# Kernel tuning notes

Measured on AMD Instinct MI355X. Metric: run time of the kernel, lower is better.

## Reference

```python
import jax, jax.numpy as jnp
import numpy as np

NEG = 0.01  # leaky_relu negative slope

def leaky(x):
    return jax.nn.leaky_relu(x, NEG)

def mlp3(x, W0, b0, W1, b1, W2, b2):
    h = leaky(x @ W0 + b0)
    h = leaky(h @ W1 + b1)
    return h @ W2 + b2

B_, T_, N_FINE, F_IN = 2, 4, 64800, 78
N_COARSE, E_LAT, H, D_OUT = 842, 5894, 256, 256

def setup_inputs() -> dict:
    key = jax.random.key(0)
    ks = jax.random.split(key, 24)
    def lin(k, i, o):
        return jax.random.normal(k, (i, o), jnp.float32) * 0.02, jnp.zeros((o,), jnp.float32)
    x = jax.random.normal(ks[0], (B_, T_, N_FINE, F_IN), jnp.float32)
    # one edge per fine node: src = node index, dst = its coarse h3 cell
    edge_index = jnp.stack([jnp.arange(N_FINE, dtype=jnp.int32),
                            jax.random.randint(ks[1], (N_FINE,), 0, N_COARSE, dtype=jnp.int32)])
    edge_attr = 2.0 * jax.random.uniform(ks[2], (N_FINE, 2), jnp.float32) - 1.0  # [sin d, cos d]
    latent_edge_index = jax.random.randint(ks[3], (2, E_LAT), 0, N_COARSE, dtype=jnp.int32)
    latent_edge_attr = 2.0 * jax.random.uniform(ks[4], (E_LAT, 2), jnp.float32) - 1.0
    h3_nodes = jax.random.normal(ks[5], (N_COARSE, F_IN), jnp.float32) * 0.02
    eW0, eb0 = lin(ks[6], 2 * F_IN + 2, H); eW1, eb1 = lin(ks[7], H, H); eW2, eb2 = lin(ks[8], H, D_OUT)
    nW0, nb0 = lin(ks[9], F_IN + D_OUT, H); nW1, nb1 = lin(ks[10], H, H); nW2, nb2 = lin(ks[11], H, D_OUT)
    rW0, rb0 = lin(ks[12], 2, H); rW1, rb1 = lin(ks[13], H, H); rW2, rb2 = lin(ks[14], H, D_OUT)
    rWs, rbs = lin(ks[15], 2, D_OUT)
    return dict(x=x, edge_index=edge_index, edge_attr=edge_attr,
                latent_edge_index=latent_edge_index, latent_edge_attr=latent_edge_attr,
                h3_nodes=h3_nodes,
                eW0=eW0, eb0=eb0, eW1=eW1, eb1=eb1, eW2=eW2, eb2=eb2,
                nW0=nW0, nb0=nb0, nW1=nW1, nb1=nb1, nW2=nW2, nb2=nb2,
                rW0=rW0, rb0=rb0, rW1=rW1, rb1=rb1, rW2=rW2, rb2=rb2,
                rWs=rWs, rbs=rbs)

def reference(x, edge_index, edge_attr, latent_edge_index, latent_edge_attr, h3_nodes,
              eW0, eb0, eW1, eb1, eW2, eb2,
              nW0, nb0, nW1, nb1, nW2, nb2,
              rW0, rb0, rW1, rb1, rW2, rb2, rWs, rbs):
    b, t, n, f = x.shape
    B = b * t
    xf = x.reshape(B, n, f)                      # (b t) n f
    src, dst = edge_index[0], edge_index[1]      # [E]
    nc = h3_nodes.shape[0]
    E = src.shape[0]
    # --- edge MLP: gather src fine feats, dst latent feats, edge attrs ---
    e_in = jnp.concatenate([
        xf[:, src],                                          # [B,E,f]
        jnp.broadcast_to(h3_nodes[dst][None], (B, E, f)),    # [B,E,f]
        jnp.broadcast_to(edge_attr[None], (B, E, 2)),        # [B,E,2]
    ], axis=-1)
    msgs = mlp3(e_in, eW0, eb0, eW1, eb1, eW2, eb2)          # [B,E,D]
    # --- scatter-sum to coarse nodes ---
    agg = jax.vmap(lambda m: jax.ops.segment_sum(m, dst, num_segments=nc))(msgs)  # [B,nc,D]
    # --- node MLP on concat(latent nodes, aggregated messages) ---
    n_in = jnp.concatenate([jnp.broadcast_to(h3_nodes[None], (B, nc, f)), agg], axis=-1)
    nodes = mlp3(n_in, nW0, nb0, nW1, nb1, nW2, nb2)          # [B,nc,D]
    nodes = nodes.reshape(b, t, nc, -1)
    # --- residual MLP over latent edge attrs (eval: dropout off, parametrized skip) ---
    h = leaky(latent_edge_attr @ rW0 + rb0)
    h = leaky(h @ rW1 + rb1)
    attrs = h @ rW2 + rb2 + (latent_edge_attr @ rWs + rbs)
    return (nodes, latent_edge_index, attrs)
```

## Files before the change

### kernel.cpp

```cpp
#include <hip/hip_runtime.h>

#define E_EDGES 64800
#define NC      842
#define NB      8
#define FIN     78
#define E_LAT   5894
#define NROWS_NODE (NB*NC)
#define NTILES_E 2025
#define NODE_B   421
#define TAIL_B   192

#define OUT_IDX_OFF   1724416
#define OUT_IDX_N     11788
#define OUT_ATTR_OFF  1736204

#define AGG_OFF    0
#define CNT_OFF    6897664
#define CUR_OFF    6901032
#define SSRC_OFF   6904400
#define SDST_OFF   7163600
#define SATTR_OFF  7293200
#define WPACK_OFF  7811600

#define WOFF_E0 0
#define WOFF_E1 24576
#define WOFF_E2 90112
#define WOFF_N0 155648
#define WOFF_N1 245760
#define WOFF_N2 311296
#define WOFF_R0 376832
#define WOFF_R1 385024
#define WOFF_R2 450560

#define SH   262
#define SA_N 362

typedef __bf16 bf16x8 __attribute__((ext_vector_type(8)));
typedef float  f32x4  __attribute__((ext_vector_type(4)));

__device__ __forceinline__ unsigned short f2bf(float f) {
    unsigned u = __builtin_bit_cast(unsigned, f);
    return (unsigned short)((u + 0x7fffu + ((u >> 16) & 1u)) >> 16);
}
__device__ __forceinline__ unsigned packRTZ(float lo, float hi) {
    return __builtin_amdgcn_perm(__builtin_bit_cast(unsigned, hi),
                                 __builtin_bit_cast(unsigned, lo), 0x07060302u);
}

template<int MF>
__device__ __forceinline__ void zero_acc(f32x4 (&acc)[MF][4]) {
#pragma unroll
    for (int mf = 0; mf < MF; ++mf)
#pragma unroll
        for (int nf = 0; nf < 4; ++nf)
            acc[mf][nf] = (f32x4){0.f, 0.f, 0.f, 0.f};
}

template<int MF, int NKS>
__device__ __forceinline__ void run_layer(const unsigned short* lA, int strideA,
                                          const unsigned short* Wp, int nfg0,
                                          int m15, int q, f32x4 (&acc)[MF][4]) {
    const unsigned short* wp0 = Wp + (size_t)nfg0 * 512 + (threadIdx.x & 63) * 8;
    bf16x8 bcur[4], bnxt[4];
#pragma unroll
    for (int nf = 0; nf < 4; ++nf) bcur[nf] = *(const bf16x8*)(wp0 + nf * 512);
#pragma unroll
    for (int kk = 0; kk < NKS; ++kk) {
        if (kk + 1 < NKS) {
#pragma unroll
            for (int nf = 0; nf < 4; ++nf)
                bnxt[nf] = *(const bf16x8*)(wp0 + (size_t)(kk + 1) * 16 * 512 + nf * 512);
        }
        bf16x8 a[MF];
#pragma unroll
        for (int mf = 0; mf < MF; ++mf)
            a[mf] = *(const bf16x8*)(lA + (mf * 16 + m15) * strideA + kk * 32 + q * 8);
#pragma unroll
        for (int nf = 0; nf < 4; ++nf)
#pragma unroll
            for (int mf = 0; mf < MF; ++mf)
                acc[mf][nf] = __builtin_amdgcn_mfma_f32_16x16x32_bf16(a[mf], bcur[nf], acc[mf][nf], 0, 0, 0);
#pragma unroll
        for (int nf = 0; nf < 4; ++nf) bcur[nf] = bnxt[nf];
    }
}

template<int MF>
__device__ __forceinline__ void epi_act(unsigned short* Sb, int stride, const f32x4 (&acc)[MF][4],
                                        const float* bias, int w, int m15, int q) {
#pragma unroll
    for (int nf = 0; nf < 4; ++nf) {
        int col = w * 64 + nf * 16 + m15;
        float bv = bias[col];
#pragma unroll
        for (int mf = 0; mf < MF; ++mf)
#pragma unroll
            for (int r4 = 0; r4 < 4; ++r4) {
                int row = mf * 16 + q * 4 + r4;
                float y = acc[mf][nf][r4] + bv;
                y = fmaxf(y, 0.01f * y);
                Sb[row * stride + col] = (unsigned short)(__builtin_bit_cast(unsigned, y) >> 16);
            }
    }
}

__global__ void pack_weights(const float* s0, const float* s1, const float* s2,
                             const float* s3, const float* s4, const float* s5,
                             const float* s6, const float* s7, const float* s8,
                             unsigned short* wp) {
    const int ksA[9]  = {3, 8, 8, 11, 8, 8, 1, 8, 8};
    const int kaA[9]  = {96, 256, 256, 334, 256, 256, 2, 256, 256};
    const int offA[9] = {WOFF_E0, WOFF_E1, WOFF_E2, WOFF_N0, WOFF_N1, WOFF_N2,
                         WOFF_R0, WOFF_R1, WOFF_R2};
    const float* srcs[9] = {s0, s1, s2, s3, s4, s5, s6, s7, s8};
    int rem = blockIdx.x;
    int l = 0;
    while (rem >= ksA[l] * 16) { rem -= ksA[l] * 16; ++l; }
    int kk = rem >> 4, nf = rem & 15;
    int lane = threadIdx.x >> 3, j = threadIdx.x & 7;
    int k = kk * 32 + (lane >> 4) * 8 + j;
    int n = nf * 16 + (lane & 15);
    float v = 0.f;
    if (l == 0) {
        int sr = (k < 78) ? k : ((k < 80) ? 156 + (k - 78) : -1);
        if (sr >= 0) v = s0[sr * 256 + n];
    } else {
        v = (k < kaA[l]) ? srcs[l][k * 256 + n] : 0.f;
    }
    wp[(size_t)offA[l] + (size_t)(kk * 16 + nf) * 512 + lane * 8 + j] = f2bf(v);
}

__global__ __launch_bounds__(256) void h3mm_kernel(const float* __restrict__ h3,
                                                   const float* __restrict__ eW0,
                                                   const float* __restrict__ eb0,
                                                   float* __restrict__ h3we) {
    __shared__ float hs[16][80];
    const int tid = threadIdx.x;
    const int rbase = blockIdx.x * 16;
    for (int i = tid; i < 16 * 78; i += 256) {
        int r = i / 78, k = i % 78;
        int gr = rbase + r;
        hs[r][k] = (gr < NC) ? h3[gr * FIN + k] : 0.f;
    }
    __syncthreads();
    const int c = tid;
    float acc[16];
#pragma unroll
    for (int r = 0; r < 16; ++r) acc[r] = eb0[c];
    for (int k = 0; k < 78; ++k) {
        float wv = eW0[(78 + k) * 256 + c];
#pragma unroll
        for (int r = 0; r < 16; ++r) acc[r] = fmaf(hs[r][k], wv, acc[r]);
    }
#pragma unroll
    for (int r = 0; r < 16; ++r) {
        int gr = rbase + r;
        if (gr < NC) h3we[(size_t)gr * 256 + c] = acc[r];
    }
}

__global__ void hist_kernel(const int* __restrict__ dstA, int* __restrict__ cnt) {
    int e = blockIdx.x * 256 + threadIdx.x;
    if (e < E_EDGES) atomicAdd(&cnt[dstA[e]], 1);
}
__global__ void scan_kernel(const int* __restrict__ cnt, int* __restrict__ cursor) {
    __shared__ int s[1024];
    int t = threadIdx.x;
    s[t] = (t < NC) ? cnt[t] : 0;
    __syncthreads();
    for (int d = 1; d < 1024; d <<= 1) {
        int v = (t >= d) ? s[t - d] : 0;
        __syncthreads();
        s[t] += v;
        __syncthreads();
    }
    if (t < NC) cursor[t] = (t == 0) ? 0 : s[t - 1];
}
__global__ void scatter_kernel(const int* __restrict__ srcA, const int* __restrict__ dstA,
                               const float* __restrict__ eattr, int* __restrict__ cursor,
                               int* __restrict__ ssrc, short* __restrict__ sdst,
                               float2* __restrict__ sattr) {
    int e = blockIdx.x * 256 + threadIdx.x;
    if (e < E_EDGES) {
        int d = dstA[e];
        int p = atomicAdd(&cursor[d], 1);
        ssrc[p] = srcA[e];
        sdst[p] = (short)d;
        sattr[p] = ((const float2*)eattr)[e];
    }
}

__global__ __launch_bounds__(256, 6) void edge_mlp_kernel(
    const float* __restrict__ x, const float* __restrict__ h3we,
    const float* __restrict__ eb1, const float* __restrict__ eb2,
    const unsigned short* __restrict__ wpack, const int* __restrict__ ssrc,
    const short* __restrict__ sdst, const float2* __restrict__ sattr,
    float* __restrict__ agg) {
    __shared__ __align__(16) unsigned short S[32 * SH];
    __shared__ short dstl[32];
    __shared__ unsigned char starts[36];
    __shared__ int nseg;

    const int base = blockIdx.x * 32, b = blockIdx.y;
    const int tid = threadIdx.x, lane = tid & 63, w = tid >> 6;
    const int m15 = lane & 15, q = lane >> 4;

    if (tid < 32) dstl[tid] = sdst[base + tid];
    __syncthreads();

    if (tid == 0) {
        int ns = 0; short prev = -2;
        for (int r = 0; r < 32; ++r) {
            short d = dstl[r];
            if (d != prev) { starts[ns++] = (unsigned char)r; prev = d; }
        }
        starts[ns] = 32;
        nseg = ns;
    }

    {
        const int rr = tid >> 3, j = tid & 7;
        const int eg = base + rr;
        const float* xr = x + ((size_t)b * E_EDGES + ssrc[eg]) * FIN;
        unsigned short* Sr = S + rr * SH;
#pragma unroll
        for (int t = 0; t < 6; ++t) {
            int p = j + 8 * t;
            if (p < 39) {
                float2 f = *(const float2*)(xr + 2 * p);
                *(unsigned*)(Sr + 2 * p) = packRTZ(f.x, f.y);
            } else if (p == 39) {
                float2 a2 = sattr[eg];
                *(unsigned*)(Sr + 78) = packRTZ(a2.x, a2.y);
            } else {
                *(unsigned*)(Sr + 2 * p) = 0;
            }
        }
    }
    float bnf[4];
#pragma unroll
    for (int nf = 0; nf < 4; ++nf) bnf[nf] = eb2[w * 64 + nf * 16 + m15];
    __syncthreads();

    f32x4 acc[2][4];
    zero_acc<2>(acc);
    run_layer<2, 3>(S, SH, wpack + WOFF_E0, w * 4, m15, q, acc);
    __syncthreads();
    {
#pragma unroll
        for (int mf = 0; mf < 2; ++mf)
#pragma unroll
            for (int r4 = 0; r4 < 4; ++r4) {
                int row = mf * 16 + q * 4 + r4;
                const float* hb = h3we + (size_t)dstl[row] * 256;
#pragma unroll
                for (int nf = 0; nf < 4; ++nf) {
                    int col = w * 64 + nf * 16 + m15;
                    float y = acc[mf][nf][r4] + hb[col];
                    y = fmaxf(y, 0.01f * y);
                    S[row * SH + col] = (unsigned short)(__builtin_bit_cast(unsigned, y) >> 16);
                }
            }
    }
    __syncthreads();

    zero_acc<2>(acc);
    run_layer<2, 8>(S, SH, wpack + WOFF_E1, w * 4, m15, q, acc);
    __syncthreads();
    epi_act<2>(S, SH, acc, eb1, w, m15, q);
    __syncthreads();

    zero_acc<2>(acc);
    run_layer<2, 8>(S, SH, wpack + WOFF_E2, w * 4, m15, q, acc);

    const int ns = nseg;
#pragma unroll
    for (int nf = 0; nf < 4; ++nf) {
        for (int s = 0; s < ns; ++s) {
            const int lo = starts[s], hi = starts[s + 1];
            float t = 0.f;
#pragma unroll
            for (int mf = 0; mf < 2; ++mf)
#pragma unroll
                for (int r4 = 0; r4 < 4; ++r4) {
                    int row = mf * 16 + q * 4 + r4;
                    t += (row >= lo && row < hi) ? acc[mf][nf][r4] : 0.f;
                }
            t += __shfl_xor(t, 16, 64);
            t += __shfl_xor(t, 32, 64);
            if (q == nf) {
                int dc = dstl[lo];
                atomicAdd(&agg[((size_t)b * NC + dc) * 256 + w * 64 + nf * 16 + m15],
                          t + bnf[nf] * (float)(hi - lo));
            }
        }
    }
}

__global__ __launch_bounds__(256, 4) void node_tail_kernel(
    const float* __restrict__ h3, const float* __restrict__ agg,
    const float* __restrict__ nb0, const float* __restrict__ nb1, const float* __restrict__ nb2,
    const unsigned short* __restrict__ wpack, float* __restrict__ out,
    const float* __restrict__ la, const float* __restrict__ rb0,
    const float* __restrict__ rb1, const float* __restrict__ rb2,
    const float* __restrict__ rWs, const float* __restrict__ rbs,
    const int* __restrict__ lei) {
    __shared__ __align__(16) unsigned short S[32 * SH];

    const int tid = threadIdx.x, lane = tid & 63, w = tid >> 6;
    const int m15 = lane & 15, q = lane >> 4;

    if (blockIdx.x >= NODE_B) {
        const int blk = blockIdx.x - NODE_B;
        if (blk >= 185) {
            for (int i = (blk - 185) * 256 + tid; i < OUT_IDX_N; i += 7 * 256)
                out[OUT_IDX_OFF + i] = (float)lei[i];
            return;
        }
        const int base = blk * 32;
        {
            const int rr = tid >> 3, jj = tid & 7;
            unsigned short* Sr = S + rr * SH;
            unsigned v0 = 0;
            if (jj == 0 && base + rr < E_LAT) {
                float2 f = *(const float2*)(la + (size_t)(base + rr) * 2);
                v0 = packRTZ(f.x, f.y);
            }
            *(unsigned*)(Sr + 2 * jj) = v0;
            *(unsigned*)(Sr + 2 * (jj + 8)) = 0;
        }
        __syncthreads();

        f32x4 acc[2][4];
        zero_acc<2>(acc);
        run_layer<2, 1>(S, SH, wpack + WOFF_R0, w * 4, m15, q, acc);
        __syncthreads();
        epi_act<2>(S, SH, acc, rb0, w, m15, q);
        __syncthreads();

        zero_acc<2>(acc);
        run_layer<2, 8>(S, SH, wpack + WOFF_R1, w * 4, m15, q, acc);
        __syncthreads();
        epi_act<2>(S, SH, acc, rb1, w, m15, q);
        __syncthreads();

        zero_acc<2>(acc);
        run_layer<2, 8>(S, SH, wpack + WOFF_R2, w * 4, m15, q, acc);

        float* outA = out + OUT_ATTR_OFF;
#pragma unroll
        for (int nf = 0; nf < 4; ++nf) {
            int col = w * 64 + nf * 16 + m15;
            float bv = rb2[col] + rbs[col];
            float ws0 = rWs[col], ws1 = rWs[256 + col];
#pragma unroll
            for (int mf = 0; mf < 2; ++mf)
#pragma unroll
                for (int r4 = 0; r4 < 4; ++r4) {
                    int row = mf * 16 + q * 4 + r4;
                    int e = base + row;
                    if (e < E_LAT) {
                        float v = acc[mf][nf][r4] + bv + la[e * 2] * ws0 + la[e * 2 + 1] * ws1;
                        outA[(size_t)e * 256 + col] = v;
                    }
                }
        }
        return;
    }

    const int base = blockIdx.x * 16;

    {
        const int rr = tid >> 4, l16 = tid & 15;
        const int jj = base + rr;
        const int vl = jj < NROWS_NODE;
        const int c = vl ? jj % NC : 0;
        const float* hr = h3 + c * FIN;
        const float* ar = agg + (size_t)jj * 256;
        unsigned short* Sr = S + rr * SA_N;
#pragma unroll
        for (int tt = 0; tt < 12; ++tt) {
            int p = l16 + 16 * tt;
            if (p < 39) {
                float2 f = *(const float2*)(hr + 2 * p);
                *(unsigned*)(Sr + 2 * p) = packRTZ(f.x, f.y);
            } else if (p < 167) {
                unsigned v = 0;
                if (vl) { float2 f = *(const float2*)(ar + 2 * p - 78); v = packRTZ(f.x, f.y); }
                *(unsigned*)(Sr + 2 * p) = v;
            } else if (p < 176) {
                *(unsigned*)(Sr + 2 * p) = 0;
            }
        }
    }
    __syncthreads();

    f32x4 acc[1][4];
    zero_acc<1>(acc);
    run_layer<1, 11>(S, SA_N, wpack + WOFF_N0, w * 4, m15, q, acc);
    __syncthreads();
    epi_act<1>(S, SA_N, acc, nb0, w, m15, q);
    __syncthreads();

    zero_acc<1>(acc);
    run_layer<1, 8>(S, SA_N, wpack + WOFF_N1, w * 4, m15, q, acc);
    __syncthreads();
    epi_act<1>(S, SA_N, acc, nb1, w, m15, q);
    __syncthreads();

    zero_acc<1>(acc);
    run_layer<1, 8>(S, SA_N, wpack + WOFF_N2, w * 4, m15, q, acc);

#pragma unroll
    for (int nf = 0; nf < 4; ++nf) {
        int col = w * 64 + nf * 16 + m15;
        float bv = nb2[col];
#pragma unroll
        for (int r4 = 0; r4 < 4; ++r4) {
            int jj = base + q * 4 + r4;
            if (jj < NROWS_NODE) out[(size_t)jj * 256 + col] = acc[0][nf][r4] + bv;
        }
    }
}

extern "C" void kernel_launch(void* const* d_in, const int* in_sizes, int n_in,
                              void* d_out, int out_size, void* d_ws, size_t ws_size,
                              hipStream_t stream) {
    const float* x      = (const float*)d_in[0];
    const int*   eidx   = (const int*)d_in[1];
    const float* eattr  = (const float*)d_in[2];
    const int*   lei    = (const int*)d_in[3];
    const float* la     = (const float*)d_in[4];
    const float* h3     = (const float*)d_in[5];
    const float* eW0 = (const float*)d_in[6],  *eb0 = (const float*)d_in[7];
    const float* eW1 = (const float*)d_in[8],  *eb1 = (const float*)d_in[9];
    const float* eW2 = (const float*)d_in[10], *eb2 = (const float*)d_in[11];
    const float* nW0 = (const float*)d_in[12], *nb0 = (const float*)d_in[13];
    const float* nW1 = (const float*)d_in[14], *nb1 = (const float*)d_in[15];
    const float* nW2 = (const float*)d_in[16], *nb2 = (const float*)d_in[17];
    const float* rW0 = (const float*)d_in[18], *rb0 = (const float*)d_in[19];
    const float* rW1 = (const float*)d_in[20], *rb1 = (const float*)d_in[21];
    const float* rW2 = (const float*)d_in[22], *rb2 = (const float*)d_in[23];
    const float* rWs = (const float*)d_in[24], *rbs = (const float*)d_in[25];

    char* ws = (char*)d_ws;
    float* agg    = (float*)(ws + AGG_OFF);
    int* cnt      = (int*)(ws + CNT_OFF);
    int* cur      = (int*)(ws + CUR_OFF);
    int* ssrc     = (int*)(ws + SSRC_OFF);
    short* sdst   = (short*)(ws + SDST_OFF);
    float2* sattr = (float2*)(ws + SATTR_OFF);
    unsigned short* wpack = (unsigned short*)(ws + WPACK_OFF);

    float* out = (float*)d_out;
    float* h3we = out + OUT_ATTR_OFF;

    hipMemsetAsync(d_ws, 0, CUR_OFF, stream);

    pack_weights<<<1008, 512, 0, stream>>>(eW0, eW1, eW2, nW0, nW1, nW2, rW0, rW1, rW2, wpack);
    h3mm_kernel<<<53, 256, 0, stream>>>(h3, eW0, eb0, h3we);
    hist_kernel<<<254, 256, 0, stream>>>(eidx + E_EDGES, cnt);
    scan_kernel<<<1, 1024, 0, stream>>>(cnt, cur);
    scatter_kernel<<<254, 256, 0, stream>>>(eidx, eidx + E_EDGES, eattr, cur,
                                            ssrc, sdst, sattr);
    edge_mlp_kernel<<<dim3(NTILES_E, NB), 256, 0, stream>>>(x, h3we, eb1, eb2,
                                                            wpack, ssrc, sdst, sattr, agg);
    node_tail_kernel<<<NODE_B + TAIL_B, 256, 0, stream>>>(
        h3, agg, nb0, nb1, nb2, wpack, out,
        la, rb0, rb1, rb2, rWs, rbs, lei);
}
```

Baseline: 677.4 us.

## Stream edge-MLP weights into LDS via async DMA ring and merge prep kernels

The edge MLP kernel now copies weight k-slices into a double-buffered LDS ring with global_load_lds, prefetching two steps ahead and across layer boundaries, instead of loading B fragments from global memory straight into registers. The aim is to hide weight-load latency behind MFMA work. The extra 32KB of LDS per block lowers the occupancy hint from 6 to 3 blocks per CU. Separately, pack_weights, h3mm and hist are merged into one prep launch to cut launch overhead. The hand-written vmcnt waits assume no other outstanding vector loads, so their correctness depends on the compiler's instruction ordering.

```diff
diff --git a/kernel.cpp b/kernel.cpp
--- a/kernel.cpp
+++ b/kernel.cpp
@@ -10,6 +10,11 @@
 #define NODE_B   421
 #define TAIL_B   192
 
+#define PACK_B   1008
+#define H3MM_B   27
+#define HIST_B   127
+#define PREP_B   (PACK_B + H3MM_B + HIST_B)
+
 #define OUT_IDX_OFF   1724416
 #define OUT_IDX_N     11788
 #define OUT_ATTR_OFF  1736204
@@ -32,6 +37,8 @@
 #define WOFF_R1 385024
 #define WOFF_R2 450560
 
+#define WSTEP 8192
+
 #define SH   262
 #define SA_N 362
 
@@ -47,6 +54,13 @@
                                  __builtin_bit_cast(unsigned, lo), 0x07060302u);
 }
 
+typedef const unsigned int __attribute__((address_space(1)))* gas1_t;
+typedef unsigned int __attribute__((address_space(3)))* las3_t;
+__device__ __forceinline__ void gld_lds16(const unsigned short* g, unsigned short* l) {
+    __builtin_amdgcn_global_load_lds((gas1_t)(unsigned long long)g,
+                                     (las3_t)(unsigned)(unsigned long long)l, 16, 0, 0);
+}
+
 template<int MF>
 __device__ __forceinline__ void zero_acc(f32x4 (&acc)[MF][4]) {
 #pragma unroll
@@ -54,6 +68,47 @@
 #pragma unroll
         for (int nf = 0; nf < 4; ++nf)
             acc[mf][nf] = (f32x4){0.f, 0.f, 0.f, 0.f};
+}
+
+template<int MF, int NKS, int P, bool HN>
+__device__ __forceinline__ void run_layer_dma(const unsigned short* lA,
+                                              unsigned short* Br,
+                                              const unsigned short* Wg,
+                                              const unsigned short* WgN,
+                                              int w, int lane, int m15, int q,
+                                              f32x4 (&acc)[MF][4]) {
+    const int nfg0 = w * 4;
+#pragma unroll
+    for (int kk = 0; kk < NKS; ++kk) {
+        bf16x8 a[MF];
+#pragma unroll
+        for (int mf = 0; mf < MF; ++mf)
+            a[mf] = *(const bf16x8*)(lA + (mf * 16 + m15) * SH + kk * 32 + q * 8);
+        if (HN || kk < NKS - 1) asm volatile("s_waitcnt vmcnt(4)" ::: "memory");
+        else                    asm volatile("s_waitcnt vmcnt(0)" ::: "memory");
+        const unsigned short* bs = Br + ((P + kk) & 1) * WSTEP + w * 2048 + lane * 8;
+        bf16x8 b[4];
+#pragma unroll
+        for (int nf = 0; nf < 4; ++nf) b[nf] = *(const bf16x8*)(bs + nf * 512);
+        asm volatile("s_waitcnt lgkmcnt(0)" ::: "memory");
+        __builtin_amdgcn_sched_barrier(0);
+        const int t = kk + 2;
+        const unsigned short* src =
+            (t < NKS) ? (Wg + (size_t)(t * 16 + nfg0) * 512)
+                      : (HN ? (WgN + (size_t)((t - NKS) * 16 + nfg0) * 512)
+                            : (const unsigned short*)0);
+        if (src) {
+            unsigned short* dst = Br + ((P + t) & 1) * WSTEP + w * 2048;
+#pragma unroll
+            for (int i = 0; i < 4; ++i)
+                gld_lds16(src + i * 512 + lane * 8, dst + i * 512);
+        }
+#pragma unroll
+        for (int nf = 0; nf < 4; ++nf)
+#pragma unroll
+            for (int mf = 0; mf < MF; ++mf)
+                acc[mf][nf] = __builtin_amdgcn_mfma_f32_16x16x32_bf16(a[mf], b[nf], acc[mf][nf], 0, 0, 0);
+    }
 }
 
 template<int MF, int NKS>
@@ -104,65 +159,68 @@
     }
 }
 
-__global__ void pack_weights(const float* s0, const float* s1, const float* s2,
-                             const float* s3, const float* s4, const float* s5,
-                             const float* s6, const float* s7, const float* s8,
-                             unsigned short* wp) {
-    const int ksA[9]  = {3, 8, 8, 11, 8, 8, 1, 8, 8};
-    const int kaA[9]  = {96, 256, 256, 334, 256, 256, 2, 256, 256};
-    const int offA[9] = {WOFF_E0, WOFF_E1, WOFF_E2, WOFF_N0, WOFF_N1, WOFF_N2,
-                         WOFF_R0, WOFF_R1, WOFF_R2};
-    const float* srcs[9] = {s0, s1, s2, s3, s4, s5, s6, s7, s8};
-    int rem = blockIdx.x;
-    int l = 0;
-    while (rem >= ksA[l] * 16) { rem -= ksA[l] * 16; ++l; }
-    int kk = rem >> 4, nf = rem & 15;
-    int lane = threadIdx.x >> 3, j = threadIdx.x & 7;
-    int k = kk * 32 + (lane >> 4) * 8 + j;
-    int n = nf * 16 + (lane & 15);
-    float v = 0.f;
-    if (l == 0) {
-        int sr = (k < 78) ? k : ((k < 80) ? 156 + (k - 78) : -1);
-        if (sr >= 0) v = s0[sr * 256 + n];
-    } else {
-        v = (k < kaA[l]) ? srcs[l][k * 256 + n] : 0.f;
-    }
-    wp[(size_t)offA[l] + (size_t)(kk * 16 + nf) * 512 + lane * 8 + j] = f2bf(v);
-}
-
-__global__ __launch_bounds__(256) void h3mm_kernel(const float* __restrict__ h3,
-                                                   const float* __restrict__ eW0,
-                                                   const float* __restrict__ eb0,
-                                                   float* __restrict__ h3we) {
-    __shared__ float hs[16][80];
-    const int tid = threadIdx.x;
-    const int rbase = blockIdx.x * 16;
-    for (int i = tid; i < 16 * 78; i += 256) {
-        int r = i / 78, k = i % 78;
-        int gr = rbase + r;
-        hs[r][k] = (gr < NC) ? h3[gr * FIN + k] : 0.f;
-    }
-    __syncthreads();
-    const int c = tid;
-    float acc[16];
-#pragma unroll
-    for (int r = 0; r < 16; ++r) acc[r] = eb0[c];
-    for (int k = 0; k < 78; ++k) {
-        float wv = eW0[(78 + k) * 256 + c];
-#pragma unroll
-        for (int r = 0; r < 16; ++r) acc[r] = fmaf(hs[r][k], wv, acc[r]);
-    }
-#pragma unroll
-    for (int r = 0; r < 16; ++r) {
-        int gr = rbase + r;
-        if (gr < NC) h3we[(size_t)gr * 256 + c] = acc[r];
-    }
-}
-
-__global__ void hist_kernel(const int* __restrict__ dstA, int* __restrict__ cnt) {
-    int e = blockIdx.x * 256 + threadIdx.x;
+__global__ __launch_bounds__(512) void prep_kernel(
+    const float* s0, const float* s1, const float* s2,
+    const float* s3, const float* s4, const float* s5,
+    const float* s6, const float* s7, const float* s8,
+    unsigned short* wp,
+    const float* __restrict__ h3, const float* __restrict__ eb0,
+    float* __restrict__ h3we,
+    const int* __restrict__ dstA, int* __restrict__ cnt) {
+    __shared__ float hs[32][80];
+    const int blk = blockIdx.x, tid = threadIdx.x;
+
+    if (blk < PACK_B) {
+        const int ksA[9]  = {3, 8, 8, 11, 8, 8, 1, 8, 8};
+        const int kaA[9]  = {96, 256, 256, 334, 256, 256, 2, 256, 256};
+        const int offA[9] = {WOFF_E0, WOFF_E1, WOFF_E2, WOFF_N0, WOFF_N1, WOFF_N2,
+                             WOFF_R0, WOFF_R1, WOFF_R2};
+        const float* srcs[9] = {s0, s1, s2, s3, s4, s5, s6, s7, s8};
+        int rem = blk;
+        int l = 0;
+        while (rem >= ksA[l] * 16) { rem -= ksA[l] * 16; ++l; }
+        int kk = rem >> 4, nf = rem & 15;
+        int lane = tid >> 3, j = tid & 7;
+        int k = kk * 32 + (lane >> 4) * 8 + j;
+        int n = nf * 16 + (lane & 15);
+        float v = 0.f;
+        if (l == 0) {
+            int sr = (k < 78) ? k : ((k < 80) ? 156 + (k - 78) : -1);
+            if (sr >= 0) v = s0[sr * 256 + n];
+        } else {
+            v = (k < kaA[l]) ? srcs[l][k * 256 + n] : 0.f;
+        }
+        wp[(size_t)offA[l] + (size_t)(kk * 16 + nf) * 512 + lane * 8 + j] = f2bf(v);
+        return;
+    }
+    if (blk < PACK_B + H3MM_B) {
+        const int rbase = (blk - PACK_B) * 32;
+        for (int i = tid; i < 32 * 78; i += 512) {
+            int r = i / 78, k = i % 78;
+            int gr = rbase + r;
+            hs[r][k] = (gr < NC) ? h3[gr * FIN + k] : 0.f;
+        }
+        __syncthreads();
+        const int c = tid & 255, rh = tid >> 8;
+        float acc[16];
+#pragma unroll
+        for (int r = 0; r < 16; ++r) acc[r] = eb0[c];
+        for (int k = 0; k < 78; ++k) {
+            float wv = s0[(78 + k) * 256 + c];
+#pragma unroll
+            for (int r = 0; r < 16; ++r) acc[r] = fmaf(hs[rh * 16 + r][k], wv, acc[r]);
+        }
+#pragma unroll
+        for (int r = 0; r < 16; ++r) {
+            int gr = rbase + rh * 16 + r;
+            if (gr < NC) h3we[(size_t)gr * 256 + c] = acc[r];
+        }
+        return;
+    }
+    int e = (blk - PACK_B - H3MM_B) * 512 + tid;
     if (e < E_EDGES) atomicAdd(&cnt[dstA[e]], 1);
 }
+
 __global__ void scan_kernel(const int* __restrict__ cnt, int* __restrict__ cursor) {
     __shared__ int s[1024];
     int t = threadIdx.x;
@@ -190,13 +248,14 @@
     }
 }
 
-__global__ __launch_bounds__(256, 6) void edge_mlp_kernel(
+__global__ __launch_bounds__(256, 3) void edge_mlp_kernel(
     const float* __restrict__ x, const float* __restrict__ h3we,
     const float* __restrict__ eb1, const float* __restrict__ eb2,
     const unsigned short* __restrict__ wpack, const int* __restrict__ ssrc,
     const short* __restrict__ sdst, const float2* __restrict__ sattr,
     float* __restrict__ agg) {
     __shared__ __align__(16) unsigned short S[32 * SH];
+    __shared__ __align__(16) unsigned short Bring[2 * WSTEP];
     __shared__ short dstl[32];
     __shared__ unsigned char starts[36];
     __shared__ int nseg;
@@ -216,6 +275,18 @@
         }
         starts[ns] = 32;
         nseg = ns;
+    }
+
+    {
+        const int nfg0 = w * 4;
+#pragma unroll
+        for (int t = 0; t < 2; ++t) {
+            const unsigned short* sp = wpack + WOFF_E0 + (size_t)(t * 16 + nfg0) * 512 + lane * 8;
+            unsigned short* dp = Bring + t * WSTEP + w * 2048;
+#pragma unroll
+            for (int i = 0; i < 4; ++i)
+                gld_lds16(sp + i * 512, dp + i * 512);
+        }
     }
 
     {
@@ -244,7 +315,8 @@
 
     f32x4 acc[2][4];
     zero_acc<2>(acc);
-    run_layer<2, 3>(S, SH, wpack + WOFF_E0, w * 4, m15, q, acc);
+    run_layer_dma<2, 3, 0, true>(S, Bring, wpack + WOFF_E0, wpack + WOFF_E1,
+                                 w, lane, m15, q, acc);
     __syncthreads();
     {
 #pragma unroll
@@ -265,13 +337,15 @@
     __syncthreads();
 
     zero_acc<2>(acc);
-    run_layer<2, 8>(S, SH, wpack + WOFF_E1, w * 4, m15, q, acc);
+    run_layer_dma<2, 8, 1, true>(S, Bring, wpack + WOFF_E1, wpack + WOFF_E2,
+                                 w, lane, m15, q, acc);
     __syncthreads();
     epi_act<2>(S, SH, acc, eb1, w, m15, q);
     __syncthreads();
 
     zero_acc<2>(acc);
-    run_layer<2, 8>(S, SH, wpack + WOFF_E2, w * 4, m15, q, acc);
+    run_layer_dma<2, 8, 1, false>(S, Bring, wpack + WOFF_E2, (const unsigned short*)0,
+                                  w, lane, m15, q, acc);
 
     const int ns = nseg;
 #pragma unroll
@@ -457,9 +531,10 @@
 
     hipMemsetAsync(d_ws, 0, CUR_OFF, stream);
 
-    pack_weights<<<1008, 512, 0, stream>>>(eW0, eW1, eW2, nW0, nW1, nW2, rW0, rW1, rW2, wpack);
-    h3mm_kernel<<<53, 256, 0, stream>>>(h3, eW0, eb0, h3we);
-    hist_kernel<<<254, 256, 0, stream>>>(eidx + E_EDGES, cnt);
+    prep_kernel<<<PREP_B, 512, 0, stream>>>(eW0, eW1, eW2, nW0, nW1, nW2,
+                                            rW0, rW1, rW2, wpack,
+                                            h3, eb0, h3we,
+                                            eidx + E_EDGES, cnt);
     scan_kernel<<<1, 1024, 0, stream>>>(cnt, cur);
     scatter_kernel<<<254, 256, 0, stream>>>(eidx, eidx + E_EDGES, eattr, cur,
                                             ssrc, sdst, sattr);
```

Result: slower. 771.7 us (+13.9%).
